# Performance work log

Hardware: AMD Instinct MI355X
Metric: run time of the kernel (lower is better)

## Reference

```python
import jax, jax.numpy as jnp
import numpy as np

# Water box constants: n_atoms=192 -> 64 oxygens (type 8) + 128 hydrogens (type 1)
N_O, N_H = 64, 128
XLIM = 6.0  # params.max_rdf_dist


def _hist(d, bins):
    """np.histogram-equivalent fixed-bin histogram of 1-D values d."""
    nb = bins.shape[0] - 1
    idx = jnp.clip(jnp.searchsorted(bins, d, side='right') - 1, 0, nb - 1)
    w = ((d >= bins[0]) & (d <= bins[-1])).astype(jnp.float32)
    return jnp.zeros((nb,), jnp.float32).at[idx].add(w)


def _pair_rdf(wrapped, idx0, idx1, lattices, bins):
    # wrapped: [T, N, 3]; replicates distance_pbc_select + histogram/RDF math
    x0 = wrapped[:, idx0]                       # [T, n0, 3] (type1 atoms)
    x1 = wrapped[:, idx1]                       # [T, n1, 3] (type2 atoms)
    # x0.repeat([1,n1,1]) vs x1.repeat_interleave(n0) == outer pairing (x1 outer, x0 inner)
    delta = jnp.abs(x0[:, None, :, :] - x1[:, :, None, :])   # [T, n1, n0, 3]
    delta = jnp.where(delta > 0.5 * lattices, delta - lattices, delta)
    s = (delta ** 2).sum(-1)                    # [T, n1, n0]
    # safe sqrt (self-pairs give exact zeros)
    d = jnp.where(s > 0, jnp.sqrt(jnp.where(s > 0, s, 1.0)), 0.0)
    T = d.shape[0]
    P = d.shape[1] * d.shape[2]
    d = d.reshape(T, P)
    hists = jax.vmap(lambda dd: _hist(dd, bins))(d)          # [T, nb]
    vol = jnp.prod(lattices)
    shell = (4.0 / 3.0) * jnp.pi * (bins[1:] ** 3 - bins[:-1] ** 3)
    # aggregate RDF over all frames (zeros fall below bins[0]=1e-6, excluded)
    Z1 = (T * P / vol) * shell
    data_rdf = hists.sum(0) / Z1
    # per-frame RDFs, renormalized to the aggregate RDF's total mass
    Z2 = (T / vol) * shell
    rdfs = hists / Z2
    rdfs = rdfs / rdfs.sum(1, keepdims=True) * data_rdf.sum()
    return rdfs.mean(0)                          # [nb]


def setup_inputs() -> dict:
    key = jax.random.key(0)
    k0, k1, k2, k3 = jax.random.split(key, 4)
    T, R, N, nb = 100, 8, 192, 600
    stacked_radii = jax.random.normal(k0, (T, R, N, 3), jnp.float32) * 5.0
    ptypes = jnp.tile(jnp.array([8, 1, 1], jnp.int32), N // 3)  # O,H,H per water
    lattices = jnp.full((3,), 12.42, jnp.float32)
    bins = jnp.asarray(np.linspace(1e-6, XLIM, nb + 1), jnp.float32)
    gt_oo = jax.random.uniform(k1, (1, nb), jnp.float32)
    gt_hh = jax.random.uniform(k2, (1, nb), jnp.float32)
    gt_ho = jax.random.uniform(k3, (1, nb), jnp.float32)
    return dict(stacked_radii=stacked_radii, ptypes=ptypes, lattices=lattices,
                bins=bins, gt_oo=gt_oo, gt_hh=gt_hh, gt_ho=gt_ho)


def reference(stacked_radii, ptypes, lattices, bins, gt_oo, gt_hh, gt_ho):
    idx_O = jnp.nonzero(ptypes == 8, size=N_O)[0]
    idx_H = jnp.nonzero(ptypes == 1, size=N_H)[0]

    def per_replica(data):                       # data: [T, N, 3]
        wrapped = data / lattices % 1 * lattices  # PBC wrap into box
        rdf_oo = _pair_rdf(wrapped, idx_O, idx_O, lattices, bins)
        rdf_hh = _pair_rdf(wrapped, idx_H, idx_H, lattices, bins)
        rdf_ho = _pair_rdf(wrapped, idx_H, idx_O, lattices, bins)
        maes = jnp.stack([
            XLIM * jnp.abs(rdf_oo[None] - gt_oo).mean(),
            XLIM * jnp.abs(rdf_hh[None] - gt_hh).mean(),
            XLIM * jnp.abs(rdf_ho[None] - gt_ho).mean(),
        ])
        return jnp.concatenate([rdf_oo, rdf_hh, rdf_ho]), maes.max()

    # [T, R, N, 3] -> [R, T, N, 3], vmap over replicas
    rdf_list, max_maes = jax.vmap(per_replica)(jnp.swapaxes(stacked_radii, 0, 1))
    return rdf_list, max_maes
```

## Files before the change

### kernel.cpp

```cpp
#include <hip/hip_runtime.h>

#define T_STEPS 100
#define R_REP   8
#define NBINS   600

__global__ __launch_bounds__(256) void rdf_fused_kernel(
    const float* __restrict__ radii,
    const float* __restrict__ lattices,
    const float* __restrict__ bins,
    float* __restrict__ acc,
    float* __restrict__ sigsum)
{
#pragma clang fp contract(off)
    __shared__ float    Tq[NBINS + 2];
    __shared__ unsigned hist3[3][4][NBINS];
    __shared__ float4   sH[128];
    __shared__ float4   sO[64];
    __shared__ float    sredw[4][3];
    __shared__ float    sInv[3];

    const int blk = blockIdx.x;
    const int r   = blk % R_REP;
    const int tid = threadIdx.x;
    const int wid = tid >> 6;

    for (int b = tid; b <= NBINS + 1; b += 256) {
        if (b <= NBINS) {
            float e = bins[b];
            unsigned u = __float_as_uint(e * e);
            while (sqrtf(__uint_as_float(u)) <  e) ++u;
            while (sqrtf(__uint_as_float(u - 1)) >= e) --u;
            Tq[b] = __uint_as_float(u);
        } else {
            unsigned u = __float_as_uint(36.0f);
            while (sqrtf(__uint_as_float(u)) <= 6.0f) ++u;
            while (sqrtf(__uint_as_float(u - 1)) > 6.0f) --u;
            Tq[NBINS + 1] = __uint_as_float(u);
        }
    }
    {
        uint4* z = (uint4*)&hist3[0][0][0];
        for (int k = tid; k < 1800; k += 256) z[k] = make_uint4(0u, 0u, 0u, 0u);
    }

    const float L0 = lattices[0], L1 = lattices[1], L2 = lattices[2];
    const float* base = radii + (size_t)blk * 576;

    if (tid < 192) {
        int isH  = (tid >= 64);
        int a    = isH ? (tid - 64) : tid;
        int atom = isH ? (3 * (a >> 1) + 1 + (a & 1)) : (3 * a);
        const float* src = base + atom * 3;
        float x = src[0], y = src[1], z = src[2];
        float qx = x / L0; float wx = (qx - floorf(qx)) * L0;
        float qy = y / L1; float wy = (qy - floorf(qy)) * L1;
        float qz = z / L2; float wz = (qz - floorf(qz)) * L2;
        float4 w4 = make_float4(wx, wy, wz, 0.0f);
        if (isH) sH[a] = w4; else sO[a] = w4;
    }
    __syncthreads();

    const float T0 = Tq[0];
    const float TG = Tq[NBINS + 1];
    const float b0f = bins[0];
    const float invstep = (float)NBINS / (6.0f - b0f);

    auto bin_pair = [&](unsigned* myh, float4 A, float4 B, unsigned w) {
#pragma clang fp contract(off)
        float dx = fabsf(A.x - B.x); dx = fminf(dx, fabsf(dx - L0));
        float dy = fabsf(A.y - B.y); dy = fminf(dy, fabsf(dy - L1));
        float dz = fabsf(A.z - B.z); dz = fminf(dz, fabsf(dz - L2));
        float s = dx * dx + dy * dy + dz * dz;
        if (s < T0 || s >= TG) return;
        float dhat = __builtin_amdgcn_sqrtf(s);
        int k0 = (int)((dhat - b0f) * invstep);
        if (k0 > NBINS - 1) k0 = NBINS - 1;
        float lo = Tq[k0], hi = Tq[k0 + 1];
        int bi = k0 + (int)(s >= hi) - (int)(s < lo);
        if (bi > NBINS - 1) bi = NBINS - 1;
        atomicAdd(&myh[bi], w);
    };

    unsigned* mOO = hist3[0][wid];
    unsigned* mHH = hist3[1][wid];
    unsigned* mHO = hist3[2][wid];
    {
        int i = tid & 63;
        int kbase = (tid >> 6) + 1;
        float4 A = sO[i];
#pragma unroll
        for (int it = 0; it < 8; ++it) {
            int k = kbase + it * 4;
            bin_pair(mOO, A, sO[(i + k) & 63], (k == 32) ? 1u : 2u);
        }
    }
    {
        int i = tid & 127;
        int kbase = (tid >> 7) + 1;
        float4 A = sH[i];
#pragma unroll
        for (int it = 0; it < 32; ++it) {
            int k = kbase + it * 2;
            bin_pair(mHH, A, sH[(i + k) & 127], (k == 64) ? 1u : 2u);
        }
        int jb = tid >> 7;
#pragma unroll
        for (int it = 0; it < 32; ++it)
            bin_pair(mHO, A, sO[jb + it * 2], 1u);
    }
    __syncthreads();

    float fcs[3][3];
    float invsh[3];
    float lsig0 = 0.0f, lsig1 = 0.0f, lsig2 = 0.0f;
#pragma unroll
    for (int ii = 0; ii < 3; ++ii) {
        int b = tid + ii * 256;
        if (b < NBINS) {
            float e0 = bins[b], e1 = bins[b + 1];
            float shell = 4.18879020478639053f * (e1 * e1 * e1 - e0 * e0 * e0);
            float is = 1.0f / shell;
            invsh[ii] = is;
            float f0 = (float)(hist3[0][0][b] + hist3[0][1][b] + hist3[0][2][b] + hist3[0][3][b]);
            float f1 = (float)(hist3[1][0][b] + hist3[1][1][b] + hist3[1][2][b] + hist3[1][3][b]);
            float f2 = (float)(hist3[2][0][b] + hist3[2][1][b] + hist3[2][2][b] + hist3[2][3][b]);
            fcs[ii][0] = f0; fcs[ii][1] = f1; fcs[ii][2] = f2;
            lsig0 += f0 * is; lsig1 += f1 * is; lsig2 += f2 * is;
        } else {
            fcs[ii][0] = 0.0f; fcs[ii][1] = 0.0f; fcs[ii][2] = 0.0f;
            invsh[ii] = 0.0f;
        }
    }
#pragma unroll
    for (int off = 32; off > 0; off >>= 1) {
        lsig0 += __shfl_down(lsig0, off, 64);
        lsig1 += __shfl_down(lsig1, off, 64);
        lsig2 += __shfl_down(lsig2, off, 64);
    }
    if ((tid & 63) == 0) {
        sredw[wid][0] = lsig0; sredw[wid][1] = lsig1; sredw[wid][2] = lsig2;
    }
    __syncthreads();
    if (tid < 3) {
        float sg = sredw[0][tid] + sredw[1][tid] + sredw[2][tid] + sredw[3][tid];
        sInv[tid] = 1.0f / sg;
        atomicAdd(&sigsum[r * 3 + tid], sg);
    }
    __syncthreads();

    const float i0 = sInv[0], i1 = sInv[1], i2 = sInv[2];
    float* accr = acc + (size_t)r * 3 * NBINS;
#pragma unroll
    for (int ii = 0; ii < 3; ++ii) {
        int b = tid + ii * 256;
        if (b < NBINS) {
            float f0 = fcs[ii][0], f1 = fcs[ii][1], f2 = fcs[ii][2];
            if (f0 != 0.0f) atomicAdd(&accr[0 * NBINS + b], f0 * i0);
            if (f1 != 0.0f) atomicAdd(&accr[1 * NBINS + b], f1 * i1);
            if (f2 != 0.0f) atomicAdd(&accr[2 * NBINS + b], f2 * i2);
        }
    }
}

__global__ __launch_bounds__(640) void rdf_final_kernel(
    const float* __restrict__ acc,
    const float* __restrict__ sigsum,
    const float* __restrict__ bins,
    const float* __restrict__ lattices,
    const float* __restrict__ gt_oo,
    const float* __restrict__ gt_hh,
    const float* __restrict__ gt_ho,
    float* __restrict__ out)
{
#pragma clang fp contract(off)
    __shared__ float sred[640];

    const int blk = blockIdx.x;
    const int p = blk % 3, r = blk / 3;
    const int tid = threadIdx.x;

    const float vol = lattices[0] * lattices[1] * lattices[2];
    const float Pf  = (p == 0) ? 4096.0f : ((p == 1) ? 16384.0f : 8192.0f);
    const float S   = vol / ((float)T_STEPS * Pf) * sigsum[blk];

    const float* gt = (p == 0) ? gt_oo : ((p == 1) ? gt_hh : gt_ho);
    float lacc = 0.0f;
    if (tid < NBINS) {
        float e0 = bins[tid], e1 = bins[tid + 1];
        float shell = 4.18879020478639053f * (e1 * e1 * e1 - e0 * e0 * e0);
        float v = S * (1.0f / (float)T_STEPS) * (1.0f / shell) * acc[blk * NBINS + tid];
        out[r * 1800 + p * 600 + tid] = v;
        lacc = fabsf(v - gt[tid]);
    }
    sred[tid] = lacc;
    __syncthreads();
    for (int s2 = 512; s2 > 0; s2 >>= 1) {
        if (tid < s2 && tid + s2 < 640) sred[tid] += sred[tid + s2];
        __syncthreads();
    }
    if (tid == 0) {
        float mae = 6.0f * (sred[0] / 600.0f);
        atomicMax((int*)&out[14400 + r], __float_as_int(mae));
    }
}

extern "C" void kernel_launch(void* const* d_in, const int* in_sizes, int n_in,
                              void* d_out, int out_size, void* d_ws, size_t ws_size,
                              hipStream_t stream) {
    const float* radii    = (const float*)d_in[0];
    const float* lattices = (const float*)d_in[2];
    const float* bins     = (const float*)d_in[3];
    const float* gt_oo    = (const float*)d_in[4];
    const float* gt_hh    = (const float*)d_in[5];
    const float* gt_ho    = (const float*)d_in[6];
    float* out = (float*)d_out;

    float* acc    = (float*)d_ws;
    float* sigsum = acc + 24 * NBINS;

    hipMemsetAsync(d_ws, 0, (24 * NBINS + 24) * sizeof(float), stream);

    hipLaunchKernelGGL(rdf_fused_kernel, dim3(T_STEPS * R_REP), dim3(256), 0, stream,
                       radii, lattices, bins, acc, sigsum);
    hipLaunchKernelGGL(rdf_final_kernel, dim3(24), dim3(640), 0, stream,
                       acc, sigsum, bins, lattices, gt_oo, gt_hh, gt_ho, out);
}
```

Before: 93.98 us.

## Fuse final RDF normalization into main kernel via last-block completion counter

Removes the second kernel launch by having each block increment a global done counter. The last block to finish then computes the normalized RDFs and MAEs for all 24 replica/pair groups, one wave per group. This saves a launch and its inter-kernel gap, but the tail work now runs serially on a single block of 4 waves rather than 24 blocks. It also adds threadfence and atomic-load overhead. The max MAE is now written directly instead of via atomicMax.

After: 137.4 us. +46.2%, slower.

```diff
diff --git a/kernel.cpp b/kernel.cpp
--- a/kernel.cpp
+++ b/kernel.cpp
@@ -8,8 +8,13 @@
     const float* __restrict__ radii,
     const float* __restrict__ lattices,
     const float* __restrict__ bins,
+    const float* __restrict__ gt_oo,
+    const float* __restrict__ gt_hh,
+    const float* __restrict__ gt_ho,
     float* __restrict__ acc,
-    float* __restrict__ sigsum)
+    float* __restrict__ sigsum,
+    unsigned* __restrict__ done,
+    float* __restrict__ out)
 {
 #pragma clang fp contract(off)
     __shared__ float    Tq[NBINS + 2];
@@ -18,11 +23,14 @@
     __shared__ float4   sO[64];
     __shared__ float    sredw[4][3];
     __shared__ float    sInv[3];
+    __shared__ float    smae[24];
+    __shared__ int      sIsLast;
 
     const int blk = blockIdx.x;
     const int r   = blk % R_REP;
     const int tid = threadIdx.x;
     const int wid = tid >> 6;
+    const int lane = tid & 63;
 
     for (int b = tid; b <= NBINS + 1; b += 256) {
         if (b <= NBINS) {
@@ -81,9 +89,6 @@
         atomicAdd(&myh[bi], w);
     };
 
-    unsigned* mOO = hist3[0][wid];
-    unsigned* mHH = hist3[1][wid];
-    unsigned* mHO = hist3[2][wid];
     {
         int i = tid & 63;
         int kbase = (tid >> 6) + 1;
@@ -91,7 +96,7 @@
 #pragma unroll
         for (int it = 0; it < 8; ++it) {
             int k = kbase + it * 4;
-            bin_pair(mOO, A, sO[(i + k) & 63], (k == 32) ? 1u : 2u);
+            bin_pair(hist3[0][wid], A, sO[(i + k) & 63], (k == 32) ? 1u : 2u);
         }
     }
     {
@@ -101,17 +106,16 @@
 #pragma unroll
         for (int it = 0; it < 32; ++it) {
             int k = kbase + it * 2;
-            bin_pair(mHH, A, sH[(i + k) & 127], (k == 64) ? 1u : 2u);
+            bin_pair(hist3[1][wid], A, sH[(i + k) & 127], (k == 64) ? 1u : 2u);
         }
         int jb = tid >> 7;
 #pragma unroll
         for (int it = 0; it < 32; ++it)
-            bin_pair(mHO, A, sO[jb + it * 2], 1u);
+            bin_pair(hist3[2][wid], A, sO[jb + it * 2], 1u);
     }
     __syncthreads();
 
     float fcs[3][3];
-    float invsh[3];
     float lsig0 = 0.0f, lsig1 = 0.0f, lsig2 = 0.0f;
 #pragma unroll
     for (int ii = 0; ii < 3; ++ii) {
@@ -120,7 +124,6 @@
             float e0 = bins[b], e1 = bins[b + 1];
             float shell = 4.18879020478639053f * (e1 * e1 * e1 - e0 * e0 * e0);
             float is = 1.0f / shell;
-            invsh[ii] = is;
             float f0 = (float)(hist3[0][0][b] + hist3[0][1][b] + hist3[0][2][b] + hist3[0][3][b]);
             float f1 = (float)(hist3[1][0][b] + hist3[1][1][b] + hist3[1][2][b] + hist3[1][3][b]);
             float f2 = (float)(hist3[2][0][b] + hist3[2][1][b] + hist3[2][2][b] + hist3[2][3][b]);
@@ -128,7 +131,6 @@
             lsig0 += f0 * is; lsig1 += f1 * is; lsig2 += f2 * is;
         } else {
             fcs[ii][0] = 0.0f; fcs[ii][1] = 0.0f; fcs[ii][2] = 0.0f;
-            invsh[ii] = 0.0f;
         }
     }
 #pragma unroll
@@ -137,7 +139,7 @@
         lsig1 += __shfl_down(lsig1, off, 64);
         lsig2 += __shfl_down(lsig2, off, 64);
     }
-    if ((tid & 63) == 0) {
+    if (lane == 0) {
         sredw[wid][0] = lsig0; sredw[wid][1] = lsig1; sredw[wid][2] = lsig2;
     }
     __syncthreads();
@@ -160,47 +162,41 @@
             if (f2 != 0.0f) atomicAdd(&accr[2 * NBINS + b], f2 * i2);
         }
     }
-}
-
-__global__ __launch_bounds__(640) void rdf_final_kernel(
-    const float* __restrict__ acc,
-    const float* __restrict__ sigsum,
-    const float* __restrict__ bins,
-    const float* __restrict__ lattices,
-    const float* __restrict__ gt_oo,
-    const float* __restrict__ gt_hh,
-    const float* __restrict__ gt_ho,
-    float* __restrict__ out)
-{
-#pragma clang fp contract(off)
-    __shared__ float sred[640];
-
-    const int blk = blockIdx.x;
-    const int p = blk % 3, r = blk / 3;
-    const int tid = threadIdx.x;
-
-    const float vol = lattices[0] * lattices[1] * lattices[2];
-    const float Pf  = (p == 0) ? 4096.0f : ((p == 1) ? 16384.0f : 8192.0f);
-    const float S   = vol / ((float)T_STEPS * Pf) * sigsum[blk];
-
-    const float* gt = (p == 0) ? gt_oo : ((p == 1) ? gt_hh : gt_ho);
-    float lacc = 0.0f;
-    if (tid < NBINS) {
-        float e0 = bins[tid], e1 = bins[tid + 1];
-        float shell = 4.18879020478639053f * (e1 * e1 * e1 - e0 * e0 * e0);
-        float v = S * (1.0f / (float)T_STEPS) * (1.0f / shell) * acc[blk * NBINS + tid];
-        out[r * 1800 + p * 600 + tid] = v;
-        lacc = fabsf(v - gt[tid]);
-    }
-    sred[tid] = lacc;
-    __syncthreads();
-    for (int s2 = 512; s2 > 0; s2 >>= 1) {
-        if (tid < s2 && tid + s2 < 640) sred[tid] += sred[tid + s2];
-        __syncthreads();
-    }
+
+    __syncthreads();
     if (tid == 0) {
-        float mae = 6.0f * (sred[0] / 600.0f);
-        atomicMax((int*)&out[14400 + r], __float_as_int(mae));
+        __threadfence();
+        unsigned old = atomicAdd(done, 1u);
+        sIsLast = (old == gridDim.x - 1);
+    }
+    __syncthreads();
+    if (!sIsLast) return;
+    __threadfence();
+
+    const float vol = L0 * L1 * L2;
+    for (int g = wid; g < 24; g += 4) {
+        int p = g % 3, rr = g / 3;
+        const float Pf = (p == 0) ? 4096.0f : ((p == 1) ? 16384.0f : 8192.0f);
+        float ssum = __hip_atomic_load(&sigsum[g], __ATOMIC_ACQUIRE, __HIP_MEMORY_SCOPE_AGENT);
+        const float S = vol / ((float)T_STEPS * Pf) * ssum;
+        const float* gt = (p == 0) ? gt_oo : ((p == 1) ? gt_hh : gt_ho);
+        float lacc = 0.0f;
+        for (int b = lane; b < NBINS; b += 64) {
+            float a = __hip_atomic_load(&acc[g * NBINS + b], __ATOMIC_ACQUIRE, __HIP_MEMORY_SCOPE_AGENT);
+            float e0 = bins[b], e1 = bins[b + 1];
+            float shell = 4.18879020478639053f * (e1 * e1 * e1 - e0 * e0 * e0);
+            float v = S * (1.0f / (float)T_STEPS) * (1.0f / shell) * a;
+            out[rr * 1800 + p * 600 + b] = v;
+            lacc += fabsf(v - gt[b]);
+        }
+#pragma unroll
+        for (int off = 32; off > 0; off >>= 1) lacc += __shfl_down(lacc, off, 64);
+        if (lane == 0) smae[g] = 6.0f * (lacc / 600.0f);
+    }
+    __syncthreads();
+    if (tid < R_REP) {
+        float a = smae[tid * 3 + 0], b = smae[tid * 3 + 1], c = smae[tid * 3 + 2];
+        out[14400 + tid] = fmaxf(a, fmaxf(b, c));
     }
 }
 
@@ -215,13 +211,13 @@
     const float* gt_ho    = (const float*)d_in[6];
     float* out = (float*)d_out;
 
-    float* acc    = (float*)d_ws;
-    float* sigsum = acc + 24 * NBINS;
-
-    hipMemsetAsync(d_ws, 0, (24 * NBINS + 24) * sizeof(float), stream);
+    float*    acc    = (float*)d_ws;
+    float*    sigsum = acc + 24 * NBINS;
+    unsigned* done   = (unsigned*)(sigsum + 24);
+
+    hipMemsetAsync(d_ws, 0, (24 * NBINS + 24 + 8) * sizeof(float), stream);
 
     hipLaunchKernelGGL(rdf_fused_kernel, dim3(T_STEPS * R_REP), dim3(256), 0, stream,
-                       radii, lattices, bins, acc, sigsum);
-    hipLaunchKernelGGL(rdf_final_kernel, dim3(24), dim3(640), 0, stream,
-                       acc, sigsum, bins, lattices, gt_oo, gt_hh, gt_ho, out);
+                       radii, lattices, bins, gt_oo, gt_hh, gt_ho,
+                       acc, sigsum, done, out);
 }
```
